# Kernel tuning notes

Hardware: AMD Instinct MI355X
Metric: run time of the kernel (lower is better)

The kernel has to match this reference:

```python
import jax, jax.numpy as jnp
import numpy as np

TEMPERATURE = 2.0


def _offdiag_idx(n):
    # flat indices of the off-diagonal entries of an [n, n] matrix, row-major,
    # reshaped to [n, n-1] (matches torch masked_select(~eye).view(n, n-1))
    idx = np.arange(n * n).reshape(n, n)
    return jnp.asarray(idx[~np.eye(n, dtype=bool)].reshape(n, n - 1))


def setup_inputs() -> dict:
    key = jax.random.key(0)
    k1, k2, k3, k4 = jax.random.split(key, 4)
    B, D = 256, 512
    return {
        "wt_emb": jax.random.normal(k1, (B, D), dtype=jnp.float32),
        "mt_emb": jax.random.normal(k2, (B, D), dtype=jnp.float32),
        "label_wt": jax.random.uniform(k3, (B,), dtype=jnp.float32),
        "label_mt": jax.random.uniform(k4, (B,), dtype=jnp.float32),
    }


def reference(wt_emb, mt_emb, label_wt, label_mt):
    t = TEMPERATURE
    features = jnp.concatenate([wt_emb, mt_emb], axis=0)            # [n, D]
    labels = jnp.concatenate([label_wt, label_mt], axis=0)[:, None]  # [n, 1]
    n = features.shape[0]

    # L1 label differences: [n, n]
    label_diffs = jnp.abs(labels[:, None, :] - labels[None, :, :]).sum(-1)

    # negative L2 feature distances (safe sqrt: diagonal is exactly 0)
    diff = features[:, None, :] - features[None, :, :]               # [n, n, D]
    sq = jnp.sum(diff * diff, axis=-1)                               # [n, n]
    dist = jnp.where(sq > 0, jnp.sqrt(jnp.where(sq > 0, sq, 1.0)), 0.0)
    logits = -dist / t
    logits = logits - jax.lax.stop_gradient(jnp.max(logits, axis=1, keepdims=True))
    exp_logits = jnp.exp(logits)

    # drop diagonal -> [n, n-1]
    off = _offdiag_idx(n)
    lo = logits.reshape(-1)[off]
    eo = exp_logits.reshape(-1)[off]
    ldo = label_diffs.reshape(-1)[off]

    # vectorized over positive index k: mask[i, k, j] = ld[i, j] >= ld[i, k]
    neg_mask = ldo[:, None, :] >= ldo[:, :, None]                    # [n, n-1, n-1]
    denom = jnp.sum(jnp.where(neg_mask, eo[:, None, :], 0.0), axis=-1)  # [n, n-1]
    pos_log_probs = lo - jnp.log(denom)                              # [n, n-1]
    return -jnp.sum(pos_log_probs) / (n * (n - 1))
```

## Files before the change

kernel.cpp:

```cpp
#include <hip/hip_runtime.h>


#define N 512
#define B 256
#define D 512
#define NT 512
#define NBLK (N / 2)

#define WS_SL    0
#define WS_NORM  512
#define WS_PART  1024
#define WS_FH    2048
#define WS_G     (2048 + (N * D) / 2)

typedef _Float16 half4_t  __attribute__((ext_vector_type(4)));
typedef _Float16 half8_t  __attribute__((ext_vector_type(8)));
typedef float    f32x4    __attribute__((ext_vector_type(4)));

__global__ __launch_bounds__(NT) void sort_rows_kernel(
    const float* __restrict__ wt, const float* __restrict__ mt,
    const float* __restrict__ lwt, const float* __restrict__ lmt,
    float* __restrict__ ws)
{
    const int t = threadIdx.x, b = blockIdx.x;
    __shared__ float slab[N];
    __shared__ int scnt[4];
    __shared__ float swred[NT / 64];
    slab[t] = (t < B) ? lwt[t] : lmt[t - B];
    if (t < 4) scnt[t] = 0;
    __syncthreads();

    const int jj = t >> 7, j = b * 4 + jj;
    const int c = t & 127;
    const float lj = slab[j];
    int r = 0;
    #pragma unroll
    for (int x = c * 4; x < c * 4 + 4; ++x) {
        const float v = slab[x];
        r += (v < lj || (v == lj && x < j)) ? 1 : 0;
    }
    #pragma unroll
    for (int off = 32; off > 0; off >>= 1)
        r += __shfl_down(r, off, 64);
    if ((t & 63) == 0) atomicAdd(&scnt[jj], r);
    __syncthreads();

    if (t < 4)
        ws[WS_SL + scnt[t]] = slab[b * 4 + t];

    const int rr = scnt[jj];
    const float* F = (j < B) ? (wt + (size_t)j * D) : (mt + (size_t)(j - B) * D);
    const float4 v = ((const float4*)F)[c];
    half4_t h;
    h[0] = (_Float16)v.x; h[1] = (_Float16)v.y;
    h[2] = (_Float16)v.z; h[3] = (_Float16)v.w;
    ((half4_t*)((_Float16*)(ws + WS_FH) + (size_t)rr * D))[c] = h;
    const float f0 = (float)h[0], f1 = (float)h[1];
    const float f2 = (float)h[2], f3 = (float)h[3];
    float nacc = f0 * f0 + f1 * f1 + f2 * f2 + f3 * f3;
    #pragma unroll
    for (int off = 32; off > 0; off >>= 1)
        nacc += __shfl_down(nacc, off, 64);
    if ((t & 63) == 0) swred[t >> 6] = nacc;
    __syncthreads();
    if (t < 4)
        ws[WS_NORM + scnt[t]] = swred[2 * t] + swred[2 * t + 1];
}

__global__ __launch_bounds__(256) void gram_kernel(float* __restrict__ ws)
{
    const int lane = threadIdx.x & 63;
    const int wid  = blockIdx.x * 4 + (threadIdx.x >> 6);
    const int ti = wid >> 4, tj = wid & 15;
    const int quad = lane >> 4, m = lane & 15;

    const _Float16* Fh = (const _Float16*)(ws + WS_FH);
    const _Float16* A0 = Fh + (size_t)(ti * 32 + m) * D + quad * 8;
    const _Float16* A1 = A0 + (size_t)16 * D;
    const _Float16* B0 = Fh + (size_t)(tj * 32 + m) * D + quad * 8;
    const _Float16* B1 = B0 + (size_t)16 * D;

    f32x4 acc00 = {0.f, 0.f, 0.f, 0.f};
    f32x4 acc01 = {0.f, 0.f, 0.f, 0.f};
    f32x4 acc10 = {0.f, 0.f, 0.f, 0.f};
    f32x4 acc11 = {0.f, 0.f, 0.f, 0.f};
    #pragma unroll
    for (int k0 = 0; k0 < D; k0 += 32) {
        const half8_t a0 = *(const half8_t*)(A0 + k0);
        const half8_t a1 = *(const half8_t*)(A1 + k0);
        const half8_t b0 = *(const half8_t*)(B0 + k0);
        const half8_t b1 = *(const half8_t*)(B1 + k0);
        acc00 = __builtin_amdgcn_mfma_f32_16x16x32_f16(a0, b0, acc00, 0, 0, 0);
        acc01 = __builtin_amdgcn_mfma_f32_16x16x32_f16(a0, b1, acc01, 0, 0, 0);
        acc10 = __builtin_amdgcn_mfma_f32_16x16x32_f16(a1, b0, acc10, 0, 0, 0);
        acc11 = __builtin_amdgcn_mfma_f32_16x16x32_f16(a1, b1, acc11, 0, 0, 0);
    }
    float* G = ws + WS_G;
    const int r0 = ti * 32 + quad * 4;
    const int c0 = tj * 32 + m;
    #pragma unroll
    for (int rg = 0; rg < 4; ++rg) {
        G[(size_t)(r0 + rg) * N + c0]           = acc00[rg];
        G[(size_t)(r0 + rg) * N + c0 + 16]      = acc01[rg];
        G[(size_t)(r0 + 16 + rg) * N + c0]      = acc10[rg];
        G[(size_t)(r0 + 16 + rg) * N + c0 + 16] = acc11[rg];
    }
}

__global__ __launch_bounds__(NT) void rnc_main(float* __restrict__ ws)
{
    const int b = blockIdx.x, i0 = 2 * b, i1 = 2 * b + 1;
    const int t = threadIdx.x;
    const int w = t >> 6, lane = t & 63;

    __shared__ float sl[N];
    __shared__ float snm[N];
    __shared__ __align__(16) float sp0[N];
    __shared__ __align__(16) float sf0[N];
    __shared__ __align__(16) float sp1[N];
    __shared__ __align__(16) float sf1[N];
    __shared__ float sred[NT / 64];

    sl[t]  = ws[WS_SL + t];
    snm[t] = ws[WS_NORM + t];
    __syncthreads();
    const float li0 = sl[i0], li1 = sl[i1];
    const float ni0 = snm[i0], ni1 = snm[i1];

    const float* G = ws + WS_G;
    const float g0 = G[(size_t)i0 * N + t];
    const float g1 = G[(size_t)i1 * N + t];
    const float d0 = fmaxf(ni0 + snm[t] - 2.f * g0, 0.f);
    const float d1 = fmaxf(ni1 + snm[t] - 2.f * g1, 0.f);
    const float lg0 = -0.5f * sqrtf(d0);
    const float lg1 = -0.5f * sqrtf(d1);
    float lg_acc = 0.f;
    if (t != i0) lg_acc += lg0;
    if (t != i1) lg_acc += lg1;
    const float e0 = (t == i0) ? 0.f : __expf(lg0);
    const float e1 = (t == i1) ? 0.f : __expf(lg1);
    sp0[t] = e0; sf0[t] = e0;
    sp1[t] = e1; sf1[t] = e1;
    __syncthreads();

    if (w < 4) {
        float* arr = (w == 0) ? sp0 : (w == 1) ? sf0 : (w == 2) ? sp1 : sf1;
        float4* a4 = (float4*)arr;
        float4 u0 = a4[lane * 2], u1 = a4[lane * 2 + 1];
        float v0 = u0.x, v1 = u0.y, v2 = u0.z, v3 = u0.w;
        float v4 = u1.x, v5 = u1.y, v6 = u1.z, v7 = u1.w;
        if ((w & 1) == 0) {
            v1 += v0; v2 += v1; v3 += v2; v4 += v3; v5 += v4; v6 += v5; v7 += v6;
            float x = v7;
            #pragma unroll
            for (int off = 1; off < 64; off <<= 1) {
                const float y = __shfl_up(x, off, 64);
                if (lane >= off) x += y;
            }
            float ex = __shfl_up(x, 1, 64);
            if (lane == 0) ex = 0.f;
            v0 += ex; v1 += ex; v2 += ex; v3 += ex; v4 += ex; v5 += ex; v6 += ex; v7 += ex;
        } else {
            v6 += v7; v5 += v6; v4 += v5; v3 += v4; v2 += v3; v1 += v2; v0 += v1;
            float x = v0;
            #pragma unroll
            for (int off = 1; off < 64; off <<= 1) {
                const float y = __shfl_down(x, off, 64);
                if (lane + off < 64) x += y;
            }
            float ex = __shfl_down(x, 1, 64);
            if (lane == 63) ex = 0.f;
            v0 += ex; v1 += ex; v2 += ex; v3 += ex; v4 += ex; v5 += ex; v6 += ex; v7 += ex;
        }
        a4[lane * 2]     = make_float4(v0, v1, v2, v3);
        a4[lane * 2 + 1] = make_float4(v4, v5, v6, v7);
    }
    __syncthreads();

    float local = lg_acc;
    #pragma unroll
    for (int p = 0; p < 2; ++p) {
        const int x = t;
        const int ri = p ? i1 : i0;
        const float li = p ? li1 : li0;
        const float* SP = p ? sp1 : sp0;
        const float* SF = p ? sf1 : sf0;
        if (x != ri) {
            const float th = fabsf(li - sl[x]);
            int lo = 0, hi = ri + 1;
            while (lo < hi) {
                const int mid = (lo + hi) >> 1;
                if (fabsf(li - sl[mid]) >= th) lo = mid + 1; else hi = mid;
            }
            const int a = lo;
            lo = ri + 1; hi = N;
            while (lo < hi) {
                const int mid = (lo + hi) >> 1;
                if (fabsf(li - sl[mid]) >= th) hi = mid; else lo = mid + 1;
            }
            const int bb = lo;
            const float denom = ((a > 0) ? SP[a - 1] : 0.f) + ((bb < N) ? SF[bb] : 0.f);
            local -= __logf(denom);
        }
    }

    #pragma unroll
    for (int off = 32; off > 0; off >>= 1)
        local += __shfl_down(local, off, 64);
    if (lane == 0) sred[w] = local;
    __syncthreads();
    if (t == 0) {
        float sum = 0.f;
        #pragma unroll
        for (int k = 0; k < NT / 64; ++k) sum += sred[k];
        ws[WS_PART + b] = sum;
    }
}

__global__ __launch_bounds__(NBLK) void rnc_finalize(
    const float* __restrict__ ws, float* __restrict__ out)
{
    const int t = threadIdx.x;
    __shared__ float sred[NBLK / 64];
    float v = ws[WS_PART + t];
    #pragma unroll
    for (int off = 32; off > 0; off >>= 1)
        v += __shfl_down(v, off, 64);
    if ((t & 63) == 0) sred[t >> 6] = v;
    __syncthreads();
    if (t == 0) {
        float sum = 0.f;
        #pragma unroll
        for (int k = 0; k < NBLK / 64; ++k) sum += sred[k];
        out[0] = -sum / (float)((long)N * (N - 1));
    }
}

extern "C" void kernel_launch(void* const* d_in, const int* in_sizes, int n_in,
                              void* d_out, int out_size, void* d_ws, size_t ws_size,
                              hipStream_t stream) {
    const float* wt  = (const float*)d_in[0];
    const float* mt  = (const float*)d_in[1];
    const float* lwt = (const float*)d_in[2];
    const float* lmt = (const float*)d_in[3];
    float* out = (float*)d_out;
    float* ws  = (float*)d_ws;

    sort_rows_kernel<<<128, NT, 0, stream>>>(wt, mt, lwt, lmt, ws);
    gram_kernel<<<64, 256, 0, stream>>>(ws);
    rnc_main<<<NBLK, NT, 0, stream>>>(ws);
    rnc_finalize<<<1, NBLK, 0, stream>>>(ws, out);
}
```

Measured before the change: 76.15 us.

## Fuse label ranking and fp16 conversion into gram kernel, drop sort kernel

Removes the separate sort/convert kernel. The gram kernel now reads fp32 features directly and converts them to fp16 in registers, and one extra block computes each label's rank. Norms are taken from the Gram diagonal instead of a separate pass. rnc_main scatters the exp values into sorted positions using the stored ranks and works in original row order. This saves one launch and the fp16 staging round trip, but each gram wave now reads twice the bytes in fp32 and repeats the conversion work.

```diff
diff --git a/kernel.cpp b/kernel.cpp
--- a/kernel.cpp
+++ b/kernel.cpp
@@ -8,88 +8,76 @@
 #define NBLK (N / 2)
 
 #define WS_SL    0
-#define WS_NORM  512
+#define WS_RK    512
 #define WS_PART  1024
-#define WS_FH    2048
-#define WS_G     (2048 + (N * D) / 2)
-
-typedef _Float16 half4_t  __attribute__((ext_vector_type(4)));
+#define WS_G     2048
+
 typedef _Float16 half8_t  __attribute__((ext_vector_type(8)));
 typedef float    f32x4    __attribute__((ext_vector_type(4)));
 
-__global__ __launch_bounds__(NT) void sort_rows_kernel(
+static __device__ __forceinline__ half8_t cvt8(const float* p) {
+    const float4 u = ((const float4*)p)[0];
+    const float4 v = ((const float4*)p)[1];
+    half8_t h;
+    h[0] = (_Float16)u.x; h[1] = (_Float16)u.y;
+    h[2] = (_Float16)u.z; h[3] = (_Float16)u.w;
+    h[4] = (_Float16)v.x; h[5] = (_Float16)v.y;
+    h[6] = (_Float16)v.z; h[7] = (_Float16)v.w;
+    return h;
+}
+
+__global__ __launch_bounds__(NT) void gram_kernel(
     const float* __restrict__ wt, const float* __restrict__ mt,
     const float* __restrict__ lwt, const float* __restrict__ lmt,
     float* __restrict__ ws)
 {
-    const int t = threadIdx.x, b = blockIdx.x;
-    __shared__ float slab[N];
-    __shared__ int scnt[4];
-    __shared__ float swred[NT / 64];
-    slab[t] = (t < B) ? lwt[t] : lmt[t - B];
-    if (t < 4) scnt[t] = 0;
-    __syncthreads();
-
-    const int jj = t >> 7, j = b * 4 + jj;
-    const int c = t & 127;
-    const float lj = slab[j];
-    int r = 0;
-    #pragma unroll
-    for (int x = c * 4; x < c * 4 + 4; ++x) {
-        const float v = slab[x];
-        r += (v < lj || (v == lj && x < j)) ? 1 : 0;
-    }
-    #pragma unroll
-    for (int off = 32; off > 0; off >>= 1)
-        r += __shfl_down(r, off, 64);
-    if ((t & 63) == 0) atomicAdd(&scnt[jj], r);
-    __syncthreads();
-
-    if (t < 4)
-        ws[WS_SL + scnt[t]] = slab[b * 4 + t];
-
-    const int rr = scnt[jj];
-    const float* F = (j < B) ? (wt + (size_t)j * D) : (mt + (size_t)(j - B) * D);
-    const float4 v = ((const float4*)F)[c];
-    half4_t h;
-    h[0] = (_Float16)v.x; h[1] = (_Float16)v.y;
-    h[2] = (_Float16)v.z; h[3] = (_Float16)v.w;
-    ((half4_t*)((_Float16*)(ws + WS_FH) + (size_t)rr * D))[c] = h;
-    const float f0 = (float)h[0], f1 = (float)h[1];
-    const float f2 = (float)h[2], f3 = (float)h[3];
-    float nacc = f0 * f0 + f1 * f1 + f2 * f2 + f3 * f3;
-    #pragma unroll
-    for (int off = 32; off > 0; off >>= 1)
-        nacc += __shfl_down(nacc, off, 64);
-    if ((t & 63) == 0) swred[t >> 6] = nacc;
-    __syncthreads();
-    if (t < 4)
-        ws[WS_NORM + scnt[t]] = swred[2 * t] + swred[2 * t + 1];
-}
-
-__global__ __launch_bounds__(256) void gram_kernel(float* __restrict__ ws)
-{
-    const int lane = threadIdx.x & 63;
-    const int wid  = blockIdx.x * 4 + (threadIdx.x >> 6);
+    const int t = threadIdx.x;
+
+    if (blockIdx.x == 32) {
+        __shared__ float slab[N];
+        slab[t] = (t < B) ? lwt[t] : lmt[t - B];
+        __syncthreads();
+        const float lj = slab[t];
+        int r = 0;
+        const float4* s4 = (const float4*)slab;
+        #pragma unroll 4
+        for (int x4 = 0; x4 < N / 4; ++x4) {
+            const float4 v = s4[x4];
+            const int xb = x4 * 4;
+            r += (v.x < lj || (v.x == lj && xb + 0 < t)) ? 1 : 0;
+            r += (v.y < lj || (v.y == lj && xb + 1 < t)) ? 1 : 0;
+            r += (v.z < lj || (v.z == lj && xb + 2 < t)) ? 1 : 0;
+            r += (v.w < lj || (v.w == lj && xb + 3 < t)) ? 1 : 0;
+        }
+        ws[WS_SL + r] = lj;
+        ((int*)ws)[WS_RK + t] = r;
+        return;
+    }
+
+    const int lane = t & 63;
+    const int wid  = blockIdx.x * 8 + (t >> 6);
     const int ti = wid >> 4, tj = wid & 15;
     const int quad = lane >> 4, m = lane & 15;
 
-    const _Float16* Fh = (const _Float16*)(ws + WS_FH);
-    const _Float16* A0 = Fh + (size_t)(ti * 32 + m) * D + quad * 8;
-    const _Float16* A1 = A0 + (size_t)16 * D;
-    const _Float16* B0 = Fh + (size_t)(tj * 32 + m) * D + quad * 8;
-    const _Float16* B1 = B0 + (size_t)16 * D;
+    const int ra = ti * 32 + m;
+    const int rb = tj * 32 + m;
+    const float* A0 = ((ra < B) ? (wt + (size_t)ra * D)
+                                : (mt + (size_t)(ra - B) * D)) + quad * 8;
+    const float* A1 = A0 + (size_t)16 * D;
+    const float* B0 = ((rb < B) ? (wt + (size_t)rb * D)
+                                : (mt + (size_t)(rb - B) * D)) + quad * 8;
+    const float* B1 = B0 + (size_t)16 * D;
 
     f32x4 acc00 = {0.f, 0.f, 0.f, 0.f};
     f32x4 acc01 = {0.f, 0.f, 0.f, 0.f};
     f32x4 acc10 = {0.f, 0.f, 0.f, 0.f};
     f32x4 acc11 = {0.f, 0.f, 0.f, 0.f};
-    #pragma unroll
+    #pragma unroll 2
     for (int k0 = 0; k0 < D; k0 += 32) {
-        const half8_t a0 = *(const half8_t*)(A0 + k0);
-        const half8_t a1 = *(const half8_t*)(A1 + k0);
-        const half8_t b0 = *(const half8_t*)(B0 + k0);
-        const half8_t b1 = *(const half8_t*)(B1 + k0);
+        const half8_t a0 = cvt8(A0 + k0);
+        const half8_t a1 = cvt8(A1 + k0);
+        const half8_t b0 = cvt8(B0 + k0);
+        const half8_t b1 = cvt8(B1 + k0);
         acc00 = __builtin_amdgcn_mfma_f32_16x16x32_f16(a0, b0, acc00, 0, 0, 0);
         acc01 = __builtin_amdgcn_mfma_f32_16x16x32_f16(a0, b1, acc01, 0, 0, 0);
         acc10 = __builtin_amdgcn_mfma_f32_16x16x32_f16(a1, b0, acc10, 0, 0, 0);
@@ -109,39 +97,44 @@
 
 __global__ __launch_bounds__(NT) void rnc_main(float* __restrict__ ws)
 {
-    const int b = blockIdx.x, i0 = 2 * b, i1 = 2 * b + 1;
+    const int b = blockIdx.x, j0 = 2 * b, j1 = 2 * b + 1;
     const int t = threadIdx.x;
     const int w = t >> 6, lane = t & 63;
 
     __shared__ float sl[N];
-    __shared__ float snm[N];
     __shared__ __align__(16) float sp0[N];
     __shared__ __align__(16) float sf0[N];
     __shared__ __align__(16) float sp1[N];
     __shared__ __align__(16) float sf1[N];
     __shared__ float sred[NT / 64];
-
-    sl[t]  = ws[WS_SL + t];
-    snm[t] = ws[WS_NORM + t];
-    __syncthreads();
-    const float li0 = sl[i0], li1 = sl[i1];
-    const float ni0 = snm[i0], ni1 = snm[i1];
+    __shared__ int sri[2];
+
+    sl[t] = ws[WS_SL + t];
+    const int rk = ((const int*)ws)[WS_RK + t];
+    if (t == j0) sri[0] = rk;
+    if (t == j1) sri[1] = rk;
 
     const float* G = ws + WS_G;
-    const float g0 = G[(size_t)i0 * N + t];
-    const float g1 = G[(size_t)i1 * N + t];
-    const float d0 = fmaxf(ni0 + snm[t] - 2.f * g0, 0.f);
-    const float d1 = fmaxf(ni1 + snm[t] - 2.f * g1, 0.f);
+    const float g0 = G[(size_t)j0 * N + t];
+    const float g1 = G[(size_t)j1 * N + t];
+    const float nt = G[(size_t)t * N + t];
+    const float n0 = G[(size_t)j0 * N + j0];
+    const float n1 = G[(size_t)j1 * N + j1];
+    const float d0 = fmaxf(n0 + nt - 2.f * g0, 0.f);
+    const float d1 = fmaxf(n1 + nt - 2.f * g1, 0.f);
     const float lg0 = -0.5f * sqrtf(d0);
     const float lg1 = -0.5f * sqrtf(d1);
     float lg_acc = 0.f;
-    if (t != i0) lg_acc += lg0;
-    if (t != i1) lg_acc += lg1;
-    const float e0 = (t == i0) ? 0.f : __expf(lg0);
-    const float e1 = (t == i1) ? 0.f : __expf(lg1);
-    sp0[t] = e0; sf0[t] = e0;
-    sp1[t] = e1; sf1[t] = e1;
-    __syncthreads();
+    if (t != j0) lg_acc += lg0;
+    if (t != j1) lg_acc += lg1;
+    const float e0 = (t == j0) ? 0.f : __expf(lg0);
+    const float e1 = (t == j1) ? 0.f : __expf(lg1);
+    sp0[rk] = e0; sf0[rk] = e0;
+    sp1[rk] = e1; sf1[rk] = e1;
+    __syncthreads();
+
+    const int ri0 = sri[0], ri1 = sri[1];
+    const float li0 = sl[ri0], li1 = sl[ri1];
 
     if (w < 4) {
         float* arr = (w == 0) ? sp0 : (w == 1) ? sf0 : (w == 2) ? sp1 : sf1;
@@ -181,7 +174,7 @@
     #pragma unroll
     for (int p = 0; p < 2; ++p) {
         const int x = t;
-        const int ri = p ? i1 : i0;
+        const int ri = p ? ri1 : ri0;
         const float li = p ? li1 : li0;
         const float* SP = p ? sp1 : sp0;
         const float* SF = p ? sf1 : sf0;
@@ -246,8 +239,7 @@
     float* out = (float*)d_out;
     float* ws  = (float*)d_ws;
 
-    sort_rows_kernel<<<128, NT, 0, stream>>>(wt, mt, lwt, lmt, ws);
-    gram_kernel<<<64, 256, 0, stream>>>(ws);
+    gram_kernel<<<33, NT, 0, stream>>>(wt, mt, lwt, lmt, ws);
     rnc_main<<<NBLK, NT, 0, stream>>>(ws);
     rnc_finalize<<<1, NBLK, 0, stream>>>(ws, out);
 }
```

After: 95.64 us. +25.6%, slower.
